# Kernel optimization log

Measured on AMD Instinct MI355X. Metric: run time of the kernel, lower is better.

Reference implementation:

```python
import jax, jax.numpy as jnp
import numpy as np

B, T, D, H, K, V = 2, 2048, 2048, 16, 128, 128


def _causal_conv(x, w):
    # x: [B,T,H,C], w: [H,C,4] -> depthwise causal conv, kernel size 4
    t = x.shape[1]
    xp = jnp.pad(x, ((0, 0), (3, 0), (0, 0), (0, 0)))
    return sum(xp[:, i:i + t] * w[:, :, i] for i in range(4))


def _l2norm(x):
    return x / jnp.maximum(jnp.linalg.norm(x, axis=-1, keepdims=True), 1e-12)


def _kda_scan(q, k, v, g, beta):
    # q,k: [B,T,H,K]; v: [B,T,H,V]; g: [B,T,H,K]; beta: [B,T,H]
    b, t, h, kd = q.shape
    vd = v.shape[-1]

    def step(S, inp):
        qt, kt, vt, gt, bt = inp
        S = S * jnp.exp(gt)[..., None]                       # per-key-channel decay
        err = vt - jnp.einsum('bhk,bhkv->bhv', kt, S)        # delta-rule error
        S = S + bt[..., None, None] * (kt[..., :, None] * err[..., None, :])
        ot = jnp.einsum('bhk,bhkv->bhv', qt, S)
        return S, ot

    tm = lambda a: jnp.moveaxis(a, 1, 0)
    S0 = jnp.zeros((b, h, kd, vd), q.dtype)
    _, ys = jax.lax.scan(step, S0, (tm(q), tm(k), tm(v), tm(g), tm(beta)))
    return jnp.moveaxis(ys, 0, 1)


def setup_inputs() -> dict:
    key = jax.random.key(0)
    ks = jax.random.split(key, 16)
    s = 0.02
    rng = np.random.default_rng(0)
    dt = np.exp(rng.uniform(size=H * K) * (np.log(0.1) - np.log(0.001)) + np.log(0.001)).clip(min=1e-4)
    dt_bias = (dt + np.log(-np.expm1(-dt))).astype(np.float32)
    A_log = np.log(rng.uniform(1.0, 16.0, size=H)).astype(np.float32)
    return {
        'x': jax.random.normal(ks[0], (B, T, D), jnp.float32),
        'Wq': jax.random.normal(ks[1], (H * K, D), jnp.float32) * s,
        'Wk': jax.random.normal(ks[2], (H * K, D), jnp.float32) * s,
        'Wv': jax.random.normal(ks[3], (H * V, D), jnp.float32) * s,
        'Wf1': jax.random.normal(ks[4], (V, D), jnp.float32) * s,
        'Wf2': jax.random.normal(ks[5], (H * K, V), jnp.float32) * s,
        'Wb': jax.random.normal(ks[6], (H, D), jnp.float32) * s,
        'Wg1': jax.random.normal(ks[7], (V, D), jnp.float32) * s,
        'Wg2': jax.random.normal(ks[8], (H * V, V), jnp.float32) * s,
        'bg': jnp.zeros((H * V,), jnp.float32),
        'o_norm_w': jnp.ones((V,), jnp.float32),
        'Wout': jax.random.normal(ks[9], (D, H * V), jnp.float32) * s,
        'A_log': jnp.asarray(A_log),
        'dt_bias': jnp.asarray(dt_bias),
        'qcw': jax.random.normal(ks[10], (H, K, 4), jnp.float32) * 0.1,
        'kcw': jax.random.normal(ks[11], (H, K, 4), jnp.float32) * 0.1,
        'vcw': jax.random.normal(ks[12], (H, V, 4), jnp.float32) * 0.1,
    }


def reference(x, Wq, Wk, Wv, Wf1, Wf2, Wb, Wg1, Wg2, bg, o_norm_w, Wout, A_log, dt_bias, qcw, kcw, vcw):
    b, t, d = x.shape
    h, kd = qcw.shape[0], qcw.shape[1]
    vd = vcw.shape[1]
    q = (x @ Wq.T).reshape(b, t, h, kd)
    k = (x @ Wk.T).reshape(b, t, h, kd)
    v = (x @ Wv.T).reshape(b, t, h, vd)
    q = _l2norm(jax.nn.silu(_causal_conv(q, qcw)))
    k = _l2norm(jax.nn.silu(_causal_conv(k, kcw)))
    v = jax.nn.silu(_causal_conv(v, vcw))
    g_raw = ((x @ Wf1.T) @ Wf2.T).reshape(b, t, h, kd)
    g = -jnp.exp(A_log)[None, None, :, None] * jax.nn.softplus(g_raw + dt_bias.reshape(h, kd))
    beta = jax.nn.sigmoid(x @ Wb.T)  # [B,T,H]
    y = _kda_scan(q, k, v, g, beta)  # [B,T,H,V]
    gate = ((x @ Wg1.T) @ Wg2.T + bg).reshape(b, t, h, vd)
    eps = 1.1920929e-07  # torch.finfo(float32).eps (F.rms_norm default)
    y = y * jax.lax.rsqrt(jnp.mean(y * y, axis=-1, keepdims=True) + eps) * o_norm_w
    y = y * jax.nn.sigmoid(gate)
    return y.reshape(b, t, h * vd) @ Wout.T
```

## Files before the change

kernel.cpp:

```cpp
#include <hip/hip_runtime.h>

typedef unsigned short u16;
typedef unsigned int u32;

using short8 = __attribute__((ext_vector_type(8))) short;
using f32x4  = __attribute__((ext_vector_type(4))) float;

constexpr int kB = 2, kT = 2048, kD = 2048, kH = 16, kK = 128, kV = 128;
constexpr int kM  = kB * kT;
constexpr int kHK = kH * kK;
constexpr int kHV = kH * kV;
constexpr int CC  = 16;
constexpr int NCH = kT / CC;

constexpr size_t OFF_XB    = 0;
constexpr size_t OFF_WQKV  = 16777216;
constexpr size_t OFF_QC    = 0;
constexpr size_t OFF_YF    = 0;
constexpr size_t OFF_WF1B  = 41943040;
constexpr size_t OFF_WG1B  = 42467328;
constexpr size_t OFF_WBP   = 42991616;
constexpr size_t OFF_WF2B  = 43515904;
constexpr size_t OFF_WG2B  = 44040192;
constexpr size_t OFF_FGB   = 44564480;
constexpr size_t OFF_QKVR  = 48758784;
constexpr size_t OFF_QHB   = 48758784;
constexpr size_t OFF_KBB   = 65536000;
constexpr size_t OFF_KHB   = 82313216;
constexpr size_t OFF_YGB   = 82313216;
constexpr size_t OFF_GRAW  = 99090432;
constexpr size_t OFF_LAM   = 99090432;
constexpr size_t OFF_WINV  = 101187584;
constexpr size_t OFF_MM    = 105381888;
constexpr size_t OFF_GATEB = 115867648;
constexpr size_t OFF_WOUTB = 132644864;
constexpr size_t OFF_KC    = 141033472;
constexpr size_t OFF_VT    = 174587904;
constexpr size_t OFF_GK    = 208142336;
constexpr size_t OFF_BETA  = 241696768;

__device__ __forceinline__ u16 f2bf(float f) {
  union { float f; u32 u; } a; a.f = f;
  u32 u = a.u;
  u += 0x7fffu + ((u >> 16) & 1u);
  return (u16)(u >> 16);
}
__device__ __forceinline__ float bflo(u32 u) {
  union { u32 u; float f; } a; a.u = u << 16; return a.f;
}
__device__ __forceinline__ float bfhi(u32 u) {
  union { u32 u; float f; } a; a.u = u & 0xffff0000u; return a.f;
}
__device__ __forceinline__ float sigmoidf(float x) {
  return __builtin_amdgcn_rcpf(1.0f + __expf(-x));
}

#define GL_AS1 __attribute__((address_space(1)))
#define GL_AS3 __attribute__((address_space(3)))
__device__ __forceinline__ void async_lds16(const void* g, void* l) {
  __builtin_amdgcn_global_load_lds((GL_AS1 u32*)(size_t)g,
                                   (GL_AS3 u32*)(u32)(size_t)l, 16, 0, 0);
}

__global__ __launch_bounds__(256) void cast_all(
    const float* __restrict__ x, const float* __restrict__ Wq,
    const float* __restrict__ Wk, const float* __restrict__ Wv,
    const float* __restrict__ Wout, const float* __restrict__ Wf1,
    const float* __restrict__ Wg1, const float* __restrict__ Wf2,
    const float* __restrict__ Wg2,
    u16* __restrict__ xb, u16* __restrict__ wqkv, u16* __restrict__ woutb,
    u16* __restrict__ wf1b, u16* __restrict__ wg1b, u16* __restrict__ wf2b,
    u16* __restrict__ wg2b) {
  long qi = (long)blockIdx.x * 256 + threadIdx.x;
  const float* src; u16* dst; long off;
  if (qi < 2097152)      { src = x;    dst = xb;             off = qi; }
  else if (qi < 3145728) { src = Wq;   dst = wqkv;           off = qi - 2097152; }
  else if (qi < 4194304) { src = Wk;   dst = wqkv + 4194304; off = qi - 3145728; }
  else if (qi < 5242880) { src = Wv;   dst = wqkv + 8388608; off = qi - 4194304; }
  else if (qi < 6291456) { src = Wout; dst = woutb;          off = qi - 5242880; }
  else if (qi < 6356992) { src = Wf1;  dst = wf1b;           off = qi - 6291456; }
  else if (qi < 6422528) { src = Wg1;  dst = wg1b;           off = qi - 6356992; }
  else if (qi < 6488064) { src = Wf2;  dst = wf2b;           off = qi - 6422528; }
  else                   { src = Wg2;  dst = wg2b;           off = qi - 6488064; }
  long i = off * 4;
  float4 v = *(const float4*)(src + i);
  uint2 st;
  st.x = (u32)f2bf(v.x) | ((u32)f2bf(v.y) << 16);
  st.y = (u32)f2bf(v.z) | ((u32)f2bf(v.w) << 16);
  *(uint2*)(dst + i) = st;
}

__global__ __launch_bounds__(256) void pad_wb(const float* __restrict__ Wb,
                                              u16* __restrict__ out) {
  int i = (blockIdx.x * 256 + threadIdx.x) * 4;
  int row = i >> 11;
  uint2 st; st.x = 0; st.y = 0;
  if (row < 16) {
    float4 v = *(const float4*)(Wb + i);
    st.x = (u32)f2bf(v.x) | ((u32)f2bf(v.y) << 16);
    st.y = (u32)f2bf(v.z) | ((u32)f2bf(v.w) << 16);
  }
  *(uint2*)(out + i) = st;
}

template <bool BF16OUT>
__global__ __launch_bounds__(256) void gemm_bt(const u16* __restrict__ A,
                                               const u16* __restrict__ B,
                                               void* __restrict__ Cout,
                                               int lda, int ldb, int ldc, int K) {
  __shared__ u16 As[128 * 32];
  __shared__ u16 Bs[128 * 32];
  const int tid  = threadIdx.x;
  const int lane = tid & 63;
  const int wave = tid >> 6;
  const int wm = (wave >> 1) * 64;
  const int wn = (wave & 1) * 64;
  const long row0 = (long)blockIdx.x * 128;
  const long col0 = (long)blockIdx.y * 128;
  const int srow = tid >> 2;
  const int scol = (tid & 3) * 8;
  const u16* aptr = A + (row0 + srow) * (size_t)lda + scol;
  const u16* bptr = B + (col0 + srow) * (size_t)ldb + scol;
  u16* asd  = &As[tid * 8];
  u16* asd2 = &As[2048 + tid * 8];
  u16* bsd  = &Bs[tid * 8];
  u16* bsd2 = &Bs[2048 + tid * 8];
  const int mrow = lane & 15;
  const int kq = (lane >> 4) * 8;
  f32x4 acc[4][4] = {};
  for (int k0 = 0; k0 < K; k0 += 32) {
    async_lds16(aptr, asd);
    async_lds16(aptr + (size_t)64 * lda, asd2);
    async_lds16(bptr, bsd);
    async_lds16(bptr + (size_t)64 * ldb, bsd2);
    aptr += 32; bptr += 32;
    __syncthreads();
    short8 af[4], bfr[4];
#pragma unroll
    for (int i = 0; i < 4; ++i)
      af[i] = *(const short8*)(&As[(wm + i * 16 + mrow) * 32 + kq]);
#pragma unroll
    for (int j = 0; j < 4; ++j)
      bfr[j] = *(const short8*)(&Bs[(wn + j * 16 + mrow) * 32 + kq]);
#pragma unroll
    for (int i = 0; i < 4; ++i)
#pragma unroll
      for (int j = 0; j < 4; ++j)
        acc[i][j] = __builtin_amdgcn_mfma_f32_16x16x32_bf16(af[i], bfr[j], acc[i][j], 0, 0, 0);
    __syncthreads();
  }
  const int cn = lane & 15;
  const int rq = (lane >> 4) * 4;
#pragma unroll
  for (int i = 0; i < 4; ++i)
#pragma unroll
    for (int j = 0; j < 4; ++j) {
      size_t r = (size_t)(row0 + wm + i * 16 + rq);
      size_t c = (size_t)(col0 + wn + j * 16 + cn);
#pragma unroll
      for (int rr = 0; rr < 4; ++rr) {
        if constexpr (BF16OUT)
          ((u16*)Cout)[(r + rr) * ldc + c] = f2bf(acc[i][j][rr]);
        else
          ((float*)Cout)[(r + rr) * ldc + c] = acc[i][j][rr];
      }
    }
}

__global__ __launch_bounds__(256) void convprep(
    const u16* __restrict__ qkv, const u16* __restrict__ graw,
    const u16* __restrict__ fgb,
    const float* __restrict__ qcw, const float* __restrict__ kcw,
    const float* __restrict__ vcw, const float* __restrict__ A_log,
    const float* __restrict__ dt_bias,
    float* __restrict__ qc, float* __restrict__ kc, float* __restrict__ vt,
    float* __restrict__ gdec, float* __restrict__ beta) {
  const int wid = blockIdx.x * 8 + (threadIdx.x >> 5);
  const int l32 = threadIdx.x & 31;
  const int h  = wid & 15;
  const int bt = wid >> 4;
  const int t  = bt & (kT - 1);
  const int b  = bt >> 11;
  const int c0 = l32 * 4;
  const size_t colofs = (size_t)h * kK + c0;
  const size_t rowb = (size_t)bt * 6144 + colofs;
  float wqt[4][4], wkt[4][4], wvt[4][4];
#pragma unroll
  for (int j = 0; j < 4; ++j) {
    *(float4*)wqt[j] = *(const float4*)(qcw + (colofs + j) * 4);
    *(float4*)wkt[j] = *(const float4*)(kcw + (colofs + j) * 4);
    *(float4*)wvt[j] = *(const float4*)(vcw + (colofs + j) * 4);
  }
  float qa[4] = {0.f, 0.f, 0.f, 0.f};
  float ka[4] = {0.f, 0.f, 0.f, 0.f};
  float va[4] = {0.f, 0.f, 0.f, 0.f};
#pragma unroll
  for (int i = 0; i < 4; ++i) {
    int tt = t - 3 + i;
    if (tt >= 0) {
      size_t ro = rowb - (size_t)(3 - i) * 6144;
      uint2 uq = *(const uint2*)(qkv + ro);
      uint2 uk = *(const uint2*)(qkv + ro + 2048);
      uint2 uv = *(const uint2*)(qkv + ro + 4096);
      float q0 = bflo(uq.x), q1 = bfhi(uq.x), q2 = bflo(uq.y), q3 = bfhi(uq.y);
      float k0 = bflo(uk.x), k1 = bfhi(uk.x), k2 = bflo(uk.y), k3 = bfhi(uk.y);
      float v0 = bflo(uv.x), v1 = bfhi(uv.x), v2 = bflo(uv.y), v3 = bfhi(uv.y);
      qa[0] = fmaf(q0, wqt[0][i], qa[0]); qa[1] = fmaf(q1, wqt[1][i], qa[1]);
      qa[2] = fmaf(q2, wqt[2][i], qa[2]); qa[3] = fmaf(q3, wqt[3][i], qa[3]);
      ka[0] = fmaf(k0, wkt[0][i], ka[0]); ka[1] = fmaf(k1, wkt[1][i], ka[1]);
      ka[2] = fmaf(k2, wkt[2][i], ka[2]); ka[3] = fmaf(k3, wkt[3][i], ka[3]);
      va[0] = fmaf(v0, wvt[0][i], va[0]); va[1] = fmaf(v1, wvt[1][i], va[1]);
      va[2] = fmaf(v2, wvt[2][i], va[2]); va[3] = fmaf(v3, wvt[3][i], va[3]);
    }
  }
  float sq = 0.f, sk = 0.f;
#pragma unroll
  for (int j = 0; j < 4; ++j) {
    qa[j] *= sigmoidf(qa[j]);
    ka[j] *= sigmoidf(ka[j]);
    va[j] *= sigmoidf(va[j]);
    sq = fmaf(qa[j], qa[j], sq);
    sk = fmaf(ka[j], ka[j], sk);
  }
#pragma unroll
  for (int m = 1; m < 32; m <<= 1) {
    sq += __shfl_xor(sq, m);
    sk += __shfl_xor(sk, m);
  }
  float qinv = __builtin_amdgcn_rcpf(fmaxf(__builtin_amdgcn_sqrtf(sq), 1e-12f));
  float kinv = __builtin_amdgcn_rcpf(fmaxf(__builtin_amdgcn_sqrtf(sk), 1e-12f));
  const int bh = b * kH + h;
  const size_t outb = ((size_t)bh * kT + t) * kK + c0;
  *(float4*)(qc + outb) =
      make_float4(qa[0] * qinv, qa[1] * qinv, qa[2] * qinv, qa[3] * qinv);
  *(float4*)(kc + outb) =
      make_float4(ka[0] * kinv, ka[1] * kinv, ka[2] * kinv, ka[3] * kinv);
  const size_t vtb = ((size_t)(bh * 8 + (c0 >> 4)) * kT + t) * 16 + (c0 & 15);
  *(float4*)(vt + vtb) = make_float4(va[0], va[1], va[2], va[3]);
  uint2 ug = *(const uint2*)(graw + (size_t)bt * kHK + colofs);
  float Ae = __expf(A_log[h]);
  float4 db = *(const float4*)(dt_bias + colofs);
  float g0 = bflo(ug.x) + db.x;
  float g1 = bfhi(ug.x) + db.y;
  float g2 = bflo(ug.y) + db.z;
  float g3 = bfhi(ug.y) + db.w;
  float sp0 = (g0 > 15.f) ? g0 : __logf(1.f + __expf(g0));
  float sp1 = (g1 > 15.f) ? g1 : __logf(1.f + __expf(g1));
  float sp2 = (g2 > 15.f) ? g2 : __logf(1.f + __expf(g2));
  float sp3 = (g3 > 15.f) ? g3 : __logf(1.f + __expf(g3));
  *(float4*)(gdec + outb) = make_float4(-Ae * sp0, -Ae * sp1, -Ae * sp2, -Ae * sp3);
  if (l32 == 0) {
    float bv = bflo((u32)fgb[(size_t)bt * 384 + 256 + h]);
    beta[(size_t)bh * kT + t] = sigmoidf(bv);
  }
}

__global__ __launch_bounds__(256) void kda_p1(
    const float* __restrict__ qc, const float* __restrict__ kc,
    const float* __restrict__ gk, const float* __restrict__ betap,
    u16* __restrict__ qhb, u16* __restrict__ khb, u16* __restrict__ kbt,
    float* __restrict__ lamC, float* __restrict__ winv,
    float* __restrict__ mmat) {
  __shared__ float kL[CC][132], qL[CC][132], gL[CC][132];
  __shared__ float As[CC][CC], Ms[CC][CC];
  __shared__ float bet[CC];
  const int tid = threadIdx.x;
  const int bh = blockIdx.x >> 7;
  const int ch = blockIdx.x & 127;
  const size_t base = ((size_t)bh * kT + ch * CC) * kK;
  const int e = tid * 8;
  const int t = e >> 7, k = e & 127;
  {
    *(float4*)&kL[t][k]     = *(const float4*)(kc + base + e);
    *(float4*)&kL[t][k + 4] = *(const float4*)(kc + base + e + 4);
    *(float4*)&qL[t][k]     = *(const float4*)(qc + base + e);
    *(float4*)&qL[t][k + 4] = *(const float4*)(qc + base + e + 4);
    *(float4*)&gL[t][k]     = *(const float4*)(gk + base + e);
    *(float4*)&gL[t][k + 4] = *(const float4*)(gk + base + e + 4);
    if (tid < CC) bet[tid] = betap[(size_t)bh * kT + ch * CC + tid];
  }
  __syncthreads();
  if (tid < kK) {
    float a = gL[0][tid];
#pragma unroll
    for (int tt = 1; tt < CC; ++tt) { a += gL[tt][tid]; gL[tt][tid] = a; }
  }
  __syncthreads();
  float khr[8], qhr[8], kbw[8];
  u16 kbv[8];
  u32 pk[4] = {0,0,0,0}, pq[4] = {0,0,0,0};
#pragma unroll
  for (int j = 0; j < 8; ++j) {
    float G  = gL[t][k + j];
    float GC = gL[CC - 1][k + j];
    float eg = __expf(G);
    float kh = kL[t][k + j] * eg;
    float qh = qL[t][k + j] * eg;
    float kb = kL[t][k + j] * __expf(GC - G);
    u16 a = f2bf(kh), b_ = f2bf(qh), c = f2bf(kb);
    pk[j >> 1] |= ((u32)a)  << (16 * (j & 1));
    pq[j >> 1] |= ((u32)b_) << (16 * (j & 1));
    kbv[j] = c;
    khr[j] = bflo(a);
    qhr[j] = bflo(b_);
    kbw[j] = bflo((u32)c) * __expf(-GC);
  }
  *(uint4*)(khb + base + e) = *(uint4*)pk;
  *(uint4*)(qhb + base + e) = *(uint4*)pq;
  {
    const size_t kb2 = ((size_t)bh * NCH + ch) * (size_t)(kK * CC) +
                       (size_t)k * CC + t;
#pragma unroll
    for (int j = 0; j < 8; ++j) kbt[kb2 + (size_t)j * CC] = kbv[j];
  }
  if (tid < kK)
    lamC[((size_t)bh * NCH + ch) * kK + tid] = __expf(gL[CC - 1][tid]);
  __syncthreads();
#pragma unroll
  for (int j = 0; j < 8; ++j) {
    kL[t][k + j] = khr[j];
    qL[t][k + j] = qhr[j];
    gL[t][k + j] = kbw[j];
  }
  __syncthreads();
  {
    const int t2 = tid >> 4, s = tid & 15;
    float av = 0.f, mv = 0.f;
    for (int kk = 0; kk < kK; ++kk) {
      float w = gL[s][kk];
      av = fmaf(kL[t2][kk], w, av);
      mv = fmaf(qL[t2][kk], w, mv);
    }
    As[t2][s] = (s < t2)  ? av : 0.f;
    Ms[t2][s] = (s <= t2) ? mv : 0.f;
  }
  __syncthreads();
  if (tid < CC) {
    const int s = tid;
    float x[CC];
#pragma unroll
    for (int tt = 0; tt < CC; ++tt) {
      float sum = 0.f;
      for (int r = 0; r < tt; ++r) sum += As[tt][r] * x[r];
      x[tt] = ((tt == s) ? bet[tt] : 0.f) - bet[tt] * sum;
    }
    const size_t wb = ((size_t)bh * NCH + ch) * 256;
#pragma unroll
    for (int tt = 0; tt < CC; ++tt) winv[wb + tt * 16 + s] = x[tt];
  }
  mmat[((size_t)bh * NCH + ch) * 256 + tid] = Ms[tid >> 4][tid & 15];
}

__global__ __launch_bounds__(256) void kda_p2(
    const u16* __restrict__ khb, const u16* __restrict__ qhb,
    const u16* __restrict__ kbt, const float* __restrict__ lamC,
    const float* __restrict__ winv, const float* __restrict__ mmat,
    const float* __restrict__ vt, float* __restrict__ yf) {
  __shared__ u16 khs[2][CC][136];
  __shared__ u16 qhs[2][CC][136];
  __shared__ u16 kbs[2][kK][40];
  __shared__ float vsx[2][CC][9];
  __shared__ float wsx[2][CC][17];
  __shared__ float msx[2][CC][17];
  __shared__ float lamx[2][kK];
  __shared__ u16 s0h[CC][136];
  __shared__ u16 s0l[CC][136];
  __shared__ float pd[4][CC][17];
  __shared__ float qd[4][CC][17];
  __shared__ float t1r[CC][9];
  __shared__ float ufx[CC][9];
  __shared__ u16 ush[CC][40];
  __shared__ u16 usl[CC][40];
  const int tid = threadIdx.x;
  const int w = tid >> 6, lane = tid & 63;
  const int m15 = lane & 15, q = lane >> 4, q8 = q * 8;
  const int blk = blockIdx.x;
  const int bh = (blk & 7) + ((blk >> 7) << 3);
  const int vs = (blk >> 3) & 15;
  const int cb = vs * 8;
  for (int i = tid; i < CC * 136 / 2; i += 256) { ((u32*)s0h)[i] = 0; ((u32*)s0l)[i] = 0; }
  for (int i = tid; i < 2 * kK * 40 / 2; i += 256) ((u32*)kbs)[i] = 0;
  for (int i = tid; i < CC * 40 / 2; i += 256) { ((u32*)ush)[i] = 0; ((u32*)usl)[i] = 0; }

  uint4 rkh, rqh, rkb; float rv, rw, rm, rl;
  auto loadCh = [&](int ch) {
    const size_t cbase = ((size_t)bh * kT + ch * CC) * kK;
    rkh = *(const uint4*)(khb + cbase + tid * 8);
    rqh = *(const uint4*)(qhb + cbase + tid * 8);
    rkb = *(const uint4*)(kbt + ((size_t)bh * NCH + ch) * (size_t)(kK * CC) + tid * 8);
    rv  = (tid < CC * 8)
            ? vt[((size_t)(bh * 8 + (vs >> 1)) * kT + ch * CC + (tid >> 3)) * 16 +
                 (vs & 1) * 8 + (tid & 7)]
            : 0.f;
    const size_t sm = (size_t)bh * NCH + ch;
    rw  = winv[sm * 256 + tid];
    rm  = mmat[sm * 256 + tid];
    rl  = (tid < kK) ? lamC[sm * kK + tid] : 0.f;
  };
  auto writeStage = [&](int b) {
    const int tr = tid >> 4, tc = (tid & 15) * 8;
    *(uint4*)&khs[b][tr][tc] = rkh;
    *(uint4*)&qhs[b][tr][tc] = rqh;
    *(uint4*)&kbs[b][tid >> 1][(tid & 1) * 8] = rkb;
    if (tid < CC * 8) vsx[b][tid >> 3][tid & 7] = rv;
    wsx[b][tr][tid & 15] = rw;
    msx[b][tr][tid & 15] = rm;
    if (tid < kK) lamx[b][tid] = rl;
  };

  f32x4 St[2] = {};
  loadCh(0);
  for (int ch = 0; ch < NCH; ++ch) {
    const int b = ch & 1;
    writeStage(b);
    if (ch + 1 < NCH) loadCh(ch + 1);
    __syncthreads();
    short8 aK = *(const short8*)&khs[b][m15][w * 32 + q8];
    short8 aQ = *(const short8*)&qhs[b][m15][w * 32 + q8];
    short8 sH = *(const short8*)&s0h[m15][w * 32 + q8];
    short8 sL = *(const short8*)&s0l[m15][w * 32 + q8];
    f32x4 z = {0.f, 0.f, 0.f, 0.f};
    f32x4 P  = __builtin_amdgcn_mfma_f32_16x16x32_bf16(aK, sL, z, 0, 0, 0);
    P        = __builtin_amdgcn_mfma_f32_16x16x32_bf16(aK, sH, P, 0, 0, 0);
    f32x4 Qp = __builtin_amdgcn_mfma_f32_16x16x32_bf16(aQ, sL, z, 0, 0, 0);
    Qp       = __builtin_amdgcn_mfma_f32_16x16x32_bf16(aQ, sH, Qp, 0, 0, 0);
#pragma unroll
    for (int r = 0; r < 4; ++r) {
      pd[w][q * 4 + r][m15] = P[r];
      qd[w][q * 4 + r][m15] = Qp[r];
    }
    __syncthreads();
    const int tt = tid >> 3, vv = tid & 7;
    float qs = 0.f;
    if (tid < 128) {
      float t1 = vsx[b][tt][vv] -
                 ((pd[0][tt][vv] + pd[1][tt][vv]) + (pd[2][tt][vv] + pd[3][tt][vv]));
      qs = (qd[0][tt][vv] + qd[1][tt][vv]) + (qd[2][tt][vv] + qd[3][tt][vv]);
      t1r[tt][vv] = t1;
    }
    __syncthreads();
    if (tid < 128) {
      float u = 0.f;
#pragma unroll
      for (int s = 0; s < CC; ++s) u = fmaf(wsx[b][tt][s], t1r[s][vv], u);
      ufx[tt][vv] = u;
      u16 uh = f2bf(u);
      ush[vv][tt] = uh;
      usl[vv][tt] = f2bf(u - bflo(uh));
    }
    __syncthreads();
    if (tid < 128) {
      float o = qs;
#pragma unroll
      for (int s = 0; s < CC; ++s) o = fmaf(msx[b][tt][s], ufx[s][vv], o);
      yf[((size_t)bh * kT + ch * CC + tt) * kV + cb + vv] = o;
    }
    short8 bH = *(const short8*)&ush[m15][q8];
    short8 bL = *(const short8*)&usl[m15][q8];
#pragma unroll
    for (int j = 0; j < 2; ++j) {
      const int kt = w * 32 + j * 16;
      f32x4 S = St[j];
#pragma unroll
      for (int r = 0; r < 4; ++r) S[r] *= lamx[b][kt + q * 4 + r];
      short8 aB = *(const short8*)&kbs[b][kt + m15][q8];
      S = __builtin_amdgcn_mfma_f32_16x16x32_bf16(aB, bL, S, 0, 0, 0);
      S = __builtin_amdgcn_mfma_f32_16x16x32_bf16(aB, bH, S, 0, 0, 0);
      St[j] = S;
      u16 h0 = f2bf(S[0]), h1 = f2bf(S[1]), h2 = f2bf(S[2]), h3 = f2bf(S[3]);
      uint2 hw; hw.x = (u32)h0 | ((u32)h1 << 16); hw.y = (u32)h2 | ((u32)h3 << 16);
      *(uint2*)&s0h[m15][kt + q * 4] = hw;
      uint2 lw;
      lw.x = (u32)f2bf(S[0] - bflo(h0)) | ((u32)f2bf(S[1] - bflo(h1)) << 16);
      lw.y = (u32)f2bf(S[2] - bflo(h2)) | ((u32)f2bf(S[3] - bflo(h3)) << 16);
      *(uint2*)&s0l[m15][kt + q * 4] = lw;
    }
  }
}

__global__ __launch_bounds__(256) void postk(
    const float* __restrict__ yf, const u16* __restrict__ gateb,
    const float* __restrict__ bg, const float* __restrict__ onw,
    u16* __restrict__ ygb) {
  const int wid  = blockIdx.x * 4 + (threadIdx.x >> 6);
  const int lane = threadIdx.x & 63;
  const int h  = wid & 15;
  const int bt = wid >> 4;
  const int t  = bt & (kT - 1);
  const int b  = bt >> 11;
  const int v0 = lane * 2;
  const size_t yi = ((size_t)(b * kH + h) * kT + t) * kV + v0;
  float2 yv = *(const float2*)(yf + yi);
  float s = yv.x * yv.x + yv.y * yv.y;
#pragma unroll
  for (int m = 1; m < 64; m <<= 1) s += __shfl_xor(s, m);
  float scale = rsqrtf(s * (1.0f / 128.0f) + 1.1920929e-07f);
  const size_t gi = (size_t)bt * kHV + (size_t)h * kV + v0;
  u32 ug = *(const u32*)(gateb + gi);
  float g0 = bflo(ug) + bg[h * kV + v0];
  float g1 = bfhi(ug) + bg[h * kV + v0 + 1];
  float r0 = yv.x * scale * onw[v0] * sigmoidf(g0);
  float r1 = yv.y * scale * onw[v0 + 1] * sigmoidf(g1);
  *(u32*)(ygb + gi) = (u32)f2bf(r0) | ((u32)f2bf(r1) << 16);
}

extern "C" void kernel_launch(void* const* d_in, const int* in_sizes, int n_in,
                              void* d_out, int out_size, void* d_ws, size_t ws_size,
                              hipStream_t stream) {
  (void)in_sizes; (void)n_in; (void)out_size; (void)ws_size;
  const float* x    = (const float*)d_in[0];
  const float* Wq   = (const float*)d_in[1];
  const float* Wk   = (const float*)d_in[2];
  const float* Wv   = (const float*)d_in[3];
  const float* Wf1  = (const float*)d_in[4];
  const float* Wf2  = (const float*)d_in[5];
  const float* Wb   = (const float*)d_in[6];
  const float* Wg1  = (const float*)d_in[7];
  const float* Wg2  = (const float*)d_in[8];
  const float* bg   = (const float*)d_in[9];
  const float* onw  = (const float*)d_in[10];
  const float* Wout = (const float*)d_in[11];
  const float* A_log   = (const float*)d_in[12];
  const float* dt_bias = (const float*)d_in[13];
  const float* qcw  = (const float*)d_in[14];
  const float* kcw  = (const float*)d_in[15];
  const float* vcw  = (const float*)d_in[16];

  char* ws = (char*)d_ws;
  u16* xb     = (u16*)(ws + OFF_XB);
  u16* wqkv   = (u16*)(ws + OFF_WQKV);
  u16* wf1b   = (u16*)(ws + OFF_WF1B);
  u16* wg1b   = (u16*)(ws + OFF_WG1B);
  u16* wbp    = (u16*)(ws + OFF_WBP);
  u16* wf2b   = (u16*)(ws + OFF_WF2B);
  u16* wg2b   = (u16*)(ws + OFF_WG2B);
  u16* woutb  = (u16*)(ws + OFF_WOUTB);
  u16* fgb    = (u16*)(ws + OFF_FGB);
  u16* qkvraw = (u16*)(ws + OFF_QKVR);
  u16* graw   = (u16*)(ws + OFF_GRAW);
  u16* gateb  = (u16*)(ws + OFF_GATEB);
  u16* qhb    = (u16*)(ws + OFF_QHB);
  u16* khb    = (u16*)(ws + OFF_KHB);
  u16* kbb    = (u16*)(ws + OFF_KBB);
  u16* ygb    = (u16*)(ws + OFF_YGB);
  float* qcf   = (float*)(ws + OFF_QC);
  float* kcf   = (float*)(ws + OFF_KC);
  float* vtf   = (float*)(ws + OFF_VT);
  float* gkf   = (float*)(ws + OFF_GK);
  float* betaf = (float*)(ws + OFF_BETA);
  float* yff   = (float*)(ws + OFF_YF);
  float* lamf  = (float*)(ws + OFF_LAM);
  float* winvf = (float*)(ws + OFF_WINV);
  float* mmf   = (float*)(ws + OFF_MM);

  cast_all<<<25600, 256, 0, stream>>>(x, Wq, Wk, Wv, Wout, Wf1, Wg1, Wf2, Wg2,
                                      xb, wqkv, woutb, wf1b, wg1b, wf2b, wg2b);
  pad_wb<<<(128 * 2048 / 4 + 255) / 256, 256, 0, stream>>>(Wb, wbp);

  dim3 blk(256);
  gemm_bt<true><<<dim3(kM / 128, 6144 / 128), blk, 0, stream>>>(
      xb, wqkv, qkvraw, kD, kD, 6144, kD);
  gemm_bt<true><<<dim3(kM / 128, 384 / 128), blk, 0, stream>>>(
      xb, wf1b, fgb, kD, kD, 384, kD);
  gemm_bt<true><<<dim3(kM / 128, kHK / 128), blk, 0, stream>>>(
      fgb, wf2b, graw, 384, kV, kHK, kV);
  gemm_bt<true><<<dim3(kM / 128, kHV / 128), blk, 0, stream>>>(
      fgb + 128, wg2b, gateb, 384, kV, kHV, kV);

  convprep<<<kB * kT * kH / 8, 256, 0, stream>>>(qkvraw, graw, fgb,
                                                 qcw, kcw, vcw, A_log, dt_bias,
                                                 qcf, kcf, vtf, gkf, betaf);

  kda_p1<<<32 * NCH, 256, 0, stream>>>(qcf, kcf, gkf, betaf,
                                       qhb, khb, kbb, lamf, winvf, mmf);
  kda_p2<<<512, 256, 0, stream>>>(khb, qhb, kbb, lamf, winvf, mmf, vtf, yff);

  postk<<<kB * kT * kH / 4, 256, 0, stream>>>(yff, gateb, bg, onw, ygb);

  gemm_bt<false><<<dim3(kM / 128, kD / 128), blk, 0, stream>>>(
      ygb, woutb, (float*)d_out, kHV, kHV, kD, kHV);
}
```

Before: 717.6 us.

## Rewrite recurrent KDA scan as single-wave register-resident MFMA kernel

The chunked scan kernel changes from 512 four-wave blocks with LDS staging and several barriers per chunk to 256 single-wave blocks. Each wave now owns a 16-column value slice, keeps the full 128x16 state in registers as split hi/lo bf16, and does the W and M triangular solves with 16x16x16 MFMAs instead of scalar FMA loops. kda_p1 now emits the W-inverse and M matrices pre-split into bf16 hi/lo pairs. The intent is to drop the LDS round trips and __syncthreads on the serial chunk path, and to prefetch the next chunk's loads. The cost is fewer resident waves and more per-wave serial MFMA work.

```diff
diff --git a/kernel.cpp b/kernel.cpp
--- a/kernel.cpp
+++ b/kernel.cpp
@@ -4,6 +4,7 @@
 typedef unsigned int u32;
 
 using short8 = __attribute__((ext_vector_type(8))) short;
+using s4     = __attribute__((ext_vector_type(4))) short;
 using f32x4  = __attribute__((ext_vector_type(4))) float;
 
 constexpr int kB = 2, kT = 2048, kD = 2048, kH = 16, kK = 128, kV = 128;
@@ -51,8 +52,19 @@
 __device__ __forceinline__ float bfhi(u32 u) {
   union { u32 u; float f; } a; a.u = u & 0xffff0000u; return a.f;
 }
+union BU { uint2 u; s4 s; };
+__device__ __forceinline__ s4 us(uint2 u) { BU x; x.u = u; return x.s; }
 __device__ __forceinline__ float sigmoidf(float x) {
   return __builtin_amdgcn_rcpf(1.0f + __expf(-x));
+}
+__device__ __forceinline__ f32x4 mfma16b(s4 a, s4 b, f32x4 c) {
+  return __builtin_amdgcn_mfma_f32_16x16x16bf16_1k(a, b, c, 0, 0, 0);
+}
+__device__ __forceinline__ void packhl(const f32x4& v, uint2& hw, uint2& lw) {
+  u16 h0 = f2bf(v[0]), h1 = f2bf(v[1]), h2 = f2bf(v[2]), h3 = f2bf(v[3]);
+  hw.x = (u32)h0 | ((u32)h1 << 16); hw.y = (u32)h2 | ((u32)h3 << 16);
+  lw.x = (u32)f2bf(v[0] - bflo(h0)) | ((u32)f2bf(v[1] - bflo(h1)) << 16);
+  lw.y = (u32)f2bf(v[2] - bflo(h2)) | ((u32)f2bf(v[3] - bflo(h3)) << 16);
 }
 
 #define GL_AS1 __attribute__((address_space(1)))
@@ -259,8 +271,8 @@
     const float* __restrict__ qc, const float* __restrict__ kc,
     const float* __restrict__ gk, const float* __restrict__ betap,
     u16* __restrict__ qhb, u16* __restrict__ khb, u16* __restrict__ kbt,
-    float* __restrict__ lamC, float* __restrict__ winv,
-    float* __restrict__ mmat) {
+    float* __restrict__ lamC, u16* __restrict__ whv, u16* __restrict__ wlv,
+    u16* __restrict__ mhv, u16* __restrict__ mlv) {
   __shared__ float kL[CC][132], qL[CC][132], gL[CC][132];
   __shared__ float As[CC][CC], Ms[CC][CC];
   __shared__ float bet[CC];
@@ -301,8 +313,8 @@
     pk[j >> 1] |= ((u32)a)  << (16 * (j & 1));
     pq[j >> 1] |= ((u32)b_) << (16 * (j & 1));
     kbv[j] = c;
-    khr[j] = bflo(a);
-    qhr[j] = bflo(b_);
+    khr[j] = bflo((u32)a);
+    qhr[j] = bflo((u32)b_);
     kbw[j] = bflo((u32)c) * __expf(-GC);
   }
   *(uint4*)(khb + base + e) = *(uint4*)pk;
@@ -335,6 +347,7 @@
     Ms[t2][s] = (s <= t2) ? mv : 0.f;
   }
   __syncthreads();
+  const size_t smb = ((size_t)bh * NCH + ch) * 256;
   if (tid < CC) {
     const int s = tid;
     float x[CC];
@@ -344,138 +357,122 @@
       for (int r = 0; r < tt; ++r) sum += As[tt][r] * x[r];
       x[tt] = ((tt == s) ? bet[tt] : 0.f) - bet[tt] * sum;
     }
-    const size_t wb = ((size_t)bh * NCH + ch) * 256;
-#pragma unroll
-    for (int tt = 0; tt < CC; ++tt) winv[wb + tt * 16 + s] = x[tt];
-  }
-  mmat[((size_t)bh * NCH + ch) * 256 + tid] = Ms[tid >> 4][tid & 15];
-}
-
-__global__ __launch_bounds__(256) void kda_p2(
+#pragma unroll
+    for (int tt = 0; tt < CC; ++tt) {
+      u16 xh = f2bf(x[tt]);
+      whv[smb + tt * 16 + s] = xh;
+      wlv[smb + tt * 16 + s] = f2bf(x[tt] - bflo((u32)xh));
+    }
+  }
+  {
+    float mvv = Ms[tid >> 4][tid & 15];
+    u16 mhh = f2bf(mvv);
+    mhv[smb + tid] = mhh;
+    mlv[smb + tid] = f2bf(mvv - bflo((u32)mhh));
+  }
+}
+
+__global__ __launch_bounds__(64, 1) void kda_p2(
     const u16* __restrict__ khb, const u16* __restrict__ qhb,
     const u16* __restrict__ kbt, const float* __restrict__ lamC,
-    const float* __restrict__ winv, const float* __restrict__ mmat,
+    const u16* __restrict__ whg, const u16* __restrict__ wlg,
+    const u16* __restrict__ mhg, const u16* __restrict__ mlg,
     const float* __restrict__ vt, float* __restrict__ yf) {
-  __shared__ u16 khs[2][CC][136];
-  __shared__ u16 qhs[2][CC][136];
-  __shared__ u16 kbs[2][kK][40];
-  __shared__ float vsx[2][CC][9];
-  __shared__ float wsx[2][CC][17];
-  __shared__ float msx[2][CC][17];
-  __shared__ float lamx[2][kK];
-  __shared__ u16 s0h[CC][136];
-  __shared__ u16 s0l[CC][136];
-  __shared__ float pd[4][CC][17];
-  __shared__ float qd[4][CC][17];
-  __shared__ float t1r[CC][9];
-  __shared__ float ufx[CC][9];
-  __shared__ u16 ush[CC][40];
-  __shared__ u16 usl[CC][40];
-  const int tid = threadIdx.x;
-  const int w = tid >> 6, lane = tid & 63;
-  const int m15 = lane & 15, q = lane >> 4, q8 = q * 8;
+  const int lane = threadIdx.x;
+  const int m15 = lane & 15, q = lane >> 4;
   const int blk = blockIdx.x;
-  const int bh = (blk & 7) + ((blk >> 7) << 3);
-  const int vs = (blk >> 3) & 15;
-  const int cb = vs * 8;
-  for (int i = tid; i < CC * 136 / 2; i += 256) { ((u32*)s0h)[i] = 0; ((u32*)s0l)[i] = 0; }
-  for (int i = tid; i < 2 * kK * 40 / 2; i += 256) ((u32*)kbs)[i] = 0;
-  for (int i = tid; i < CC * 40 / 2; i += 256) { ((u32*)ush)[i] = 0; ((u32*)usl)[i] = 0; }
-
-  uint4 rkh, rqh, rkb; float rv, rw, rm, rl;
-  auto loadCh = [&](int ch) {
-    const size_t cbase = ((size_t)bh * kT + ch * CC) * kK;
-    rkh = *(const uint4*)(khb + cbase + tid * 8);
-    rqh = *(const uint4*)(qhb + cbase + tid * 8);
-    rkb = *(const uint4*)(kbt + ((size_t)bh * NCH + ch) * (size_t)(kK * CC) + tid * 8);
-    rv  = (tid < CC * 8)
-            ? vt[((size_t)(bh * 8 + (vs >> 1)) * kT + ch * CC + (tid >> 3)) * 16 +
-                 (vs & 1) * 8 + (tid & 7)]
-            : 0.f;
-    const size_t sm = (size_t)bh * NCH + ch;
-    rw  = winv[sm * 256 + tid];
-    rm  = mmat[sm * 256 + tid];
-    rl  = (tid < kK) ? lamC[sm * kK + tid] : 0.f;
-  };
-  auto writeStage = [&](int b) {
-    const int tr = tid >> 4, tc = (tid & 15) * 8;
-    *(uint4*)&khs[b][tr][tc] = rkh;
-    *(uint4*)&qhs[b][tr][tc] = rqh;
-    *(uint4*)&kbs[b][tid >> 1][(tid & 1) * 8] = rkb;
-    if (tid < CC * 8) vsx[b][tid >> 3][tid & 7] = rv;
-    wsx[b][tr][tid & 15] = rw;
-    msx[b][tr][tid & 15] = rm;
-    if (tid < kK) lamx[b][tid] = rl;
-  };
-
-  f32x4 St[2] = {};
-  loadCh(0);
-  for (int ch = 0; ch < NCH; ++ch) {
-    const int b = ch & 1;
-    writeStage(b);
-    if (ch + 1 < NCH) loadCh(ch + 1);
-    __syncthreads();
-    short8 aK = *(const short8*)&khs[b][m15][w * 32 + q8];
-    short8 aQ = *(const short8*)&qhs[b][m15][w * 32 + q8];
-    short8 sH = *(const short8*)&s0h[m15][w * 32 + q8];
-    short8 sL = *(const short8*)&s0l[m15][w * 32 + q8];
-    f32x4 z = {0.f, 0.f, 0.f, 0.f};
-    f32x4 P  = __builtin_amdgcn_mfma_f32_16x16x32_bf16(aK, sL, z, 0, 0, 0);
-    P        = __builtin_amdgcn_mfma_f32_16x16x32_bf16(aK, sH, P, 0, 0, 0);
-    f32x4 Qp = __builtin_amdgcn_mfma_f32_16x16x32_bf16(aQ, sL, z, 0, 0, 0);
-    Qp       = __builtin_amdgcn_mfma_f32_16x16x32_bf16(aQ, sH, Qp, 0, 0, 0);
-#pragma unroll
-    for (int r = 0; r < 4; ++r) {
-      pd[w][q * 4 + r][m15] = P[r];
-      qd[w][q * 4 + r][m15] = Qp[r];
-    }
-    __syncthreads();
-    const int tt = tid >> 3, vv = tid & 7;
-    float qs = 0.f;
-    if (tid < 128) {
-      float t1 = vsx[b][tt][vv] -
-                 ((pd[0][tt][vv] + pd[1][tt][vv]) + (pd[2][tt][vv] + pd[3][tt][vv]));
-      qs = (qd[0][tt][vv] + qd[1][tt][vv]) + (qd[2][tt][vv] + qd[3][tt][vv]);
-      t1r[tt][vv] = t1;
-    }
-    __syncthreads();
-    if (tid < 128) {
-      float u = 0.f;
-#pragma unroll
-      for (int s = 0; s < CC; ++s) u = fmaf(wsx[b][tt][s], t1r[s][vv], u);
-      ufx[tt][vv] = u;
-      u16 uh = f2bf(u);
-      ush[vv][tt] = uh;
-      usl[vv][tt] = f2bf(u - bflo(uh));
-    }
-    __syncthreads();
-    if (tid < 128) {
-      float o = qs;
-#pragma unroll
-      for (int s = 0; s < CC; ++s) o = fmaf(msx[b][tt][s], ufx[s][vv], o);
-      yf[((size_t)bh * kT + ch * CC + tt) * kV + cb + vv] = o;
-    }
-    short8 bH = *(const short8*)&ush[m15][q8];
-    short8 bL = *(const short8*)&usl[m15][q8];
-#pragma unroll
-    for (int j = 0; j < 2; ++j) {
-      const int kt = w * 32 + j * 16;
-      f32x4 S = St[j];
-#pragma unroll
-      for (int r = 0; r < 4; ++r) S[r] *= lamx[b][kt + q * 4 + r];
-      short8 aB = *(const short8*)&kbs[b][kt + m15][q8];
-      S = __builtin_amdgcn_mfma_f32_16x16x32_bf16(aB, bL, S, 0, 0, 0);
-      S = __builtin_amdgcn_mfma_f32_16x16x32_bf16(aB, bH, S, 0, 0, 0);
-      St[j] = S;
-      u16 h0 = f2bf(S[0]), h1 = f2bf(S[1]), h2 = f2bf(S[2]), h3 = f2bf(S[3]);
-      uint2 hw; hw.x = (u32)h0 | ((u32)h1 << 16); hw.y = (u32)h2 | ((u32)h3 << 16);
-      *(uint2*)&s0h[m15][kt + q * 4] = hw;
-      uint2 lw;
-      lw.x = (u32)f2bf(S[0] - bflo(h0)) | ((u32)f2bf(S[1] - bflo(h1)) << 16);
-      lw.y = (u32)f2bf(S[2] - bflo(h2)) | ((u32)f2bf(S[3] - bflo(h3)) << 16);
-      *(uint2*)&s0l[m15][kt + q * 4] = lw;
-    }
-  }
+  const int bh = blk & 31, vs = blk >> 5;
+  const u16*  khp  = khb + (size_t)bh * (kT * kK) + (size_t)m15 * kK + 4 * q;
+  const u16*  qhp  = qhb + (size_t)bh * (kT * kK) + (size_t)m15 * kK + 4 * q;
+  const u16*  kbp  = kbt + (size_t)bh * (NCH * kK * CC) + (size_t)m15 * CC + 4 * q;
+  const float* lamp = lamC + (size_t)bh * (NCH * kK) + 4 * q;
+  const size_t smb  = (size_t)bh * (NCH * 256) + (size_t)m15 * 16 + 4 * q;
+  const float* vp  = vt + ((size_t)(bh * 8 + vs) * kT + 4 * q) * 16 + m15;
+  float*       yp  = yf + ((size_t)bh * kT + 4 * q) * kV + vs * 16 + m15;
+
+  f32x4 S[8] = {};
+  uint2 Sh[8] = {}, Sl[8] = {};
+
+  uint2 khA[8], qhA[8]; float vA[4];
+  uint2 khB2[8], qhB2[8]; float vB[4];
+
+#define LKQ(KH, QH, VV, ch) {                                                  \
+    const u16* k_ = khp + (size_t)(ch) * (CC * kK);                            \
+    const u16* q_ = qhp + (size_t)(ch) * (CC * kK);                            \
+    _Pragma("unroll") for (int j = 0; j < 8; ++j) {                            \
+      KH[j] = *(const uint2*)(k_ + 16 * j);                                    \
+      QH[j] = *(const uint2*)(q_ + 16 * j);                                    \
+    }                                                                          \
+    const float* v_ = vp + (size_t)(ch) * (CC * 16);                           \
+    _Pragma("unroll") for (int r = 0; r < 4; ++r) VV[r] = v_[16 * r];          \
+  }
+
+#define CHUNK(KH, QH, VV, KH2, QH2, VV2, ch) {                                 \
+            \
+    uint2 kb_[8]; float4 lam_[8];                                              \
+    const u16* kb0 = kbp + (size_t)(ch) * (kK * CC);                           \
+    _Pragma("unroll") for (int j = 0; j < 8; ++j)                              \
+      kb_[j] = *(const uint2*)(kb0 + 16 * j * CC);                             \
+    const float* l0 = lamp + (size_t)(ch) * kK;                                \
+    _Pragma("unroll") for (int j = 0; j < 8; ++j)                              \
+      lam_[j] = *(const float4*)(l0 + 16 * j);                                 \
+    uint2 wh_ = *(const uint2*)(whg + smb + (size_t)(ch) * 256);               \
+    uint2 wl_ = *(const uint2*)(wlg + smb + (size_t)(ch) * 256);               \
+    uint2 mh_ = *(const uint2*)(mhg + smb + (size_t)(ch) * 256);               \
+    uint2 ml_ = *(const uint2*)(mlg + smb + (size_t)(ch) * 256);               \
+           \
+    f32x4 z_ = {0.f, 0.f, 0.f, 0.f};                                           \
+    f32x4 P0 = z_, P1 = z_, Q0 = z_, Q1 = z_;                                  \
+    _Pragma("unroll") for (int j = 0; j < 4; ++j) {                            \
+      P0 = mfma16b(us(KH[j]), us(Sl[j]), P0);                                  \
+      P0 = mfma16b(us(KH[j]), us(Sh[j]), P0);                                  \
+      P1 = mfma16b(us(KH[j + 4]), us(Sl[j + 4]), P1);                          \
+      P1 = mfma16b(us(KH[j + 4]), us(Sh[j + 4]), P1);                          \
+      Q0 = mfma16b(us(QH[j]), us(Sl[j]), Q0);                                  \
+      Q0 = mfma16b(us(QH[j]), us(Sh[j]), Q0);                                  \
+      Q1 = mfma16b(us(QH[j + 4]), us(Sl[j + 4]), Q1);                          \
+      Q1 = mfma16b(us(QH[j + 4]), us(Sh[j + 4]), Q1);                          \
+    }                                                                          \
+                                        \
+    if ((ch) + 1 < NCH) LKQ(KH2, QH2, VV2, (ch) + 1);                          \
+                    \
+    f32x4 T_, Qt_;                                                             \
+    _Pragma("unroll") for (int r = 0; r < 4; ++r) {                            \
+      T_[r]  = VV[r] - (P0[r] + P1[r]);                                        \
+      Qt_[r] = Q0[r] + Q1[r];                                                  \
+    }                                                                          \
+    uint2 Thw, Tlw; packhl(T_, Thw, Tlw);                                      \
+                                                              \
+    f32x4 U_ = mfma16b(us(wh_), us(Thw), z_);                                  \
+    U_ = mfma16b(us(wh_), us(Tlw), U_);                                        \
+    U_ = mfma16b(us(wl_), us(Thw), U_);                                        \
+    uint2 Uhw, Ulw; packhl(U_, Uhw, Ulw);                                      \
+                                                   \
+    f32x4 O_ = mfma16b(us(mh_), us(Uhw), Qt_);                                 \
+    O_ = mfma16b(us(mh_), us(Ulw), O_);                                        \
+    O_ = mfma16b(us(ml_), us(Uhw), O_);                                        \
+    {                                                                          \
+      float* y_ = yp + (size_t)(ch) * (CC * kV);                               \
+      _Pragma("unroll") for (int r = 0; r < 4; ++r) y_[r * kV] = O_[r];        \
+    }                                                                          \
+      \
+    _Pragma("unroll") for (int j = 0; j < 8; ++j) {                            \
+      f32x4 Sv = S[j];                                                         \
+      _Pragma("unroll") for (int r = 0; r < 4; ++r) Sv[r] *= lam_[j][r];       \
+      Sv = mfma16b(us(kb_[j]), us(Ulw), Sv);                                   \
+      Sv = mfma16b(us(kb_[j]), us(Uhw), Sv);                                   \
+      S[j] = Sv;                                                               \
+      packhl(Sv, Sh[j], Sl[j]);                                                \
+    }                                                                          \
+  }
+
+  LKQ(khA, qhA, vA, 0);
+  for (int ch = 0; ch < NCH; ch += 2) {
+    CHUNK(khA, qhA, vA, khB2, qhB2, vB, ch);
+    CHUNK(khB2, qhB2, vB, khA, qhA, vA, ch + 1);
+  }
+#undef LKQ
+#undef CHUNK
 }
 
 __global__ __launch_bounds__(256) void postk(
@@ -543,6 +540,10 @@
   u16* khb    = (u16*)(ws + OFF_KHB);
   u16* kbb    = (u16*)(ws + OFF_KBB);
   u16* ygb    = (u16*)(ws + OFF_YGB);
+  u16* whv    = (u16*)(ws + OFF_WINV);
+  u16* wlv    = (u16*)(ws + OFF_WINV + 2097152);
+  u16* mhv    = (u16*)(ws + OFF_MM);
+  u16* mlv    = (u16*)(ws + OFF_MM + 2097152);
   float* qcf   = (float*)(ws + OFF_QC);
   float* kcf   = (float*)(ws + OFF_KC);
   float* vtf   = (float*)(ws + OFF_VT);
@@ -550,8 +551,6 @@
   float* betaf = (float*)(ws + OFF_BETA);
   float* yff   = (float*)(ws + OFF_YF);
   float* lamf  = (float*)(ws + OFF_LAM);
-  float* winvf = (float*)(ws + OFF_WINV);
-  float* mmf   = (float*)(ws + OFF_MM);
 
   cast_all<<<25600, 256, 0, stream>>>(x, Wq, Wk, Wv, Wout, Wf1, Wg1, Wf2, Wg2,
                                       xb, wqkv, woutb, wf1b, wg1b, wf2b, wg2b);
@@ -572,8 +571,10 @@
                                                  qcf, kcf, vtf, gkf, betaf);
 
   kda_p1<<<32 * NCH, 256, 0, stream>>>(qcf, kcf, gkf, betaf,
-                                       qhb, khb, kbb, lamf, winvf, mmf);
-  kda_p2<<<512, 256, 0, stream>>>(khb, qhb, kbb, lamf, winvf, mmf, vtf, yff);
+                                       qhb, khb, kbb, lamf,
+                                       whv, wlv, mhv, mlv);
+  kda_p2<<<256, 64, 0, stream>>>(khb, qhb, kbb, lamf,
+                                 whv, wlv, mhv, mlv, vtf, yff);
 
   postk<<<kB * kT * kH / 4, 256, 0, stream>>>(yff, gateb, bg, onw, ygb);
 
```

Result: slower. 783.8 us (+9.2%).

## Swizzle GEMM block order and use K=16 MFMA for chunk state update

Applied to the files above, without the earlier changes.

The GEMM kernel now remaps its linear block index with a stride-8 swizzle so neighbouring workgroups share A/B tiles in cache. In the KDA chunk kernel, the state update switches from the 16x16x32 bf16 MFMA with zero-padded K to the 16x16x16 variant, which lets the kbs and u buffers shrink to their real width and drops the zero-fill of kbs. This cuts wasted MFMA work and LDS footprint in the serial recurrence, at the cost of split LDS stores for kbs.

```diff
diff --git a/kernel.cpp b/kernel.cpp
--- a/kernel.cpp
+++ b/kernel.cpp
@@ -4,6 +4,7 @@
 typedef unsigned int u32;
 
 using short8 = __attribute__((ext_vector_type(8))) short;
+using s4     = __attribute__((ext_vector_type(4))) short;
 using f32x4  = __attribute__((ext_vector_type(4))) float;
 
 constexpr int kB = 2, kT = 2048, kD = 2048, kH = 16, kK = 128, kV = 128;
@@ -53,6 +54,9 @@
 }
 __device__ __forceinline__ float sigmoidf(float x) {
   return __builtin_amdgcn_rcpf(1.0f + __expf(-x));
+}
+__device__ __forceinline__ f32x4 mfma16b(s4 a, s4 b, f32x4 c) {
+  return __builtin_amdgcn_mfma_f32_16x16x16bf16_1k(a, b, c, 0, 0, 0);
 }
 
 #define GL_AS1 __attribute__((address_space(1)))
@@ -115,8 +119,11 @@
   const int wave = tid >> 6;
   const int wm = (wave >> 1) * 64;
   const int wn = (wave & 1) * 64;
-  const long row0 = (long)blockIdx.x * 128;
-  const long col0 = (long)blockIdx.y * 128;
+  const int nwg = (int)(gridDim.x * gridDim.y);
+  const int lin = (int)(blockIdx.y * gridDim.x + blockIdx.x);
+  const int swz = (lin & 7) * (nwg >> 3) + (lin >> 3);
+  const long row0 = (long)(swz % (int)gridDim.x) * 128;
+  const long col0 = (long)(swz / (int)gridDim.x) * 128;
   const int srow = tid >> 2;
   const int scol = (tid & 3) * 8;
   const u16* aptr = A + (row0 + srow) * (size_t)lda + scol;
@@ -301,8 +308,8 @@
     pk[j >> 1] |= ((u32)a)  << (16 * (j & 1));
     pq[j >> 1] |= ((u32)b_) << (16 * (j & 1));
     kbv[j] = c;
-    khr[j] = bflo(a);
-    qhr[j] = bflo(b_);
+    khr[j] = bflo((u32)a);
+    qhr[j] = bflo((u32)b_);
     kbw[j] = bflo((u32)c) * __expf(-GC);
   }
   *(uint4*)(khb + base + e) = *(uint4*)pk;
@@ -358,7 +365,7 @@
     const float* __restrict__ vt, float* __restrict__ yf) {
   __shared__ u16 khs[2][CC][136];
   __shared__ u16 qhs[2][CC][136];
-  __shared__ u16 kbs[2][kK][40];
+  __shared__ u16 kbs[2][kK][20];
   __shared__ float vsx[2][CC][9];
   __shared__ float wsx[2][CC][17];
   __shared__ float msx[2][CC][17];
@@ -369,8 +376,8 @@
   __shared__ float qd[4][CC][17];
   __shared__ float t1r[CC][9];
   __shared__ float ufx[CC][9];
-  __shared__ u16 ush[CC][40];
-  __shared__ u16 usl[CC][40];
+  __shared__ u16 ush[CC][20];
+  __shared__ u16 usl[CC][20];
   const int tid = threadIdx.x;
   const int w = tid >> 6, lane = tid & 63;
   const int m15 = lane & 15, q = lane >> 4, q8 = q * 8;
@@ -379,8 +386,7 @@
   const int vs = (blk >> 3) & 15;
   const int cb = vs * 8;
   for (int i = tid; i < CC * 136 / 2; i += 256) { ((u32*)s0h)[i] = 0; ((u32*)s0l)[i] = 0; }
-  for (int i = tid; i < 2 * kK * 40 / 2; i += 256) ((u32*)kbs)[i] = 0;
-  for (int i = tid; i < CC * 40 / 2; i += 256) { ((u32*)ush)[i] = 0; ((u32*)usl)[i] = 0; }
+  for (int i = tid; i < CC * 20 / 2; i += 256) { ((u32*)ush)[i] = 0; ((u32*)usl)[i] = 0; }
 
   uint4 rkh, rqh, rkb; float rv, rw, rm, rl;
   auto loadCh = [&](int ch) {
@@ -401,7 +407,9 @@
     const int tr = tid >> 4, tc = (tid & 15) * 8;
     *(uint4*)&khs[b][tr][tc] = rkh;
     *(uint4*)&qhs[b][tr][tc] = rqh;
-    *(uint4*)&kbs[b][tid >> 1][(tid & 1) * 8] = rkb;
+    u16* kd = &kbs[b][tid >> 1][(tid & 1) * 8];
+    *(uint2*)kd = make_uint2(rkb.x, rkb.y);
+    *(uint2*)(kd + 4) = make_uint2(rkb.z, rkb.w);
     if (tid < CC * 8) vsx[b][tid >> 3][tid & 7] = rv;
     wsx[b][tr][tid & 15] = rw;
     msx[b][tr][tid & 15] = rm;
@@ -455,17 +463,17 @@
       for (int s = 0; s < CC; ++s) o = fmaf(msx[b][tt][s], ufx[s][vv], o);
       yf[((size_t)bh * kT + ch * CC + tt) * kV + cb + vv] = o;
     }
-    short8 bH = *(const short8*)&ush[m15][q8];
-    short8 bL = *(const short8*)&usl[m15][q8];
+    s4 bH = *(const s4*)&ush[m15][4 * q];
+    s4 bL = *(const s4*)&usl[m15][4 * q];
 #pragma unroll
     for (int j = 0; j < 2; ++j) {
       const int kt = w * 32 + j * 16;
       f32x4 S = St[j];
 #pragma unroll
       for (int r = 0; r < 4; ++r) S[r] *= lamx[b][kt + q * 4 + r];
-      short8 aB = *(const short8*)&kbs[b][kt + m15][q8];
-      S = __builtin_amdgcn_mfma_f32_16x16x32_bf16(aB, bL, S, 0, 0, 0);
-      S = __builtin_amdgcn_mfma_f32_16x16x32_bf16(aB, bH, S, 0, 0, 0);
+      s4 aB = *(const s4*)&kbs[b][kt + m15][4 * q];
+      S = mfma16b(aB, bL, S);
+      S = mfma16b(aB, bH, S);
       St[j] = S;
       u16 h0 = f2bf(S[0]), h1 = f2bf(S[1]), h2 = f2bf(S[2]), h3 = f2bf(S[3]);
       uint2 hw; hw.x = (u32)h0 | ((u32)h1 << 16); hw.y = (u32)h2 | ((u32)h3 << 16);
```

Measured after the change: 723.4 us. Within noise of the previous version (+0.8%).
